# Optimization experiments

Hardware: AMD Instinct MI355X
Metric: run time of the kernel (lower is better)

The kernel has to match this reference:

```python
import jax, jax.numpy as jnp
import numpy as np

B, S, D = 2, 2048, 2048
NH, NKV, HD = 16, 4, 128
ROPE_BASE = 10000.0
NEG = -1e9


def _rope_tables(seq_len, dim):
    inv_freq = 1.0 / ROPE_BASE ** (jnp.arange(0, dim, 2, dtype=jnp.float32) / dim)
    t = jnp.arange(seq_len, dtype=jnp.float32)
    freqs = jnp.outer(t, inv_freq)                      # [S, dim/2]
    return jnp.cos(freqs), jnp.sin(freqs)


def _apply_rope(x, cos, sin):
    # x: [B, S, H, HD]; interleaved-pair rotation matching the original module
    x1 = x[..., ::2]
    x2 = x[..., 1::2]
    c = cos[None, :, None, :]
    s = sin[None, :, None, :]
    out1 = x1 * c - x2 * s
    out2 = x1 * s + x2 * c
    return jnp.stack([out1, out2], axis=-1).reshape(x.shape)


def setup_inputs() -> dict:
    key = jax.random.key(0)
    ks = jax.random.split(key, 5)
    x = jax.random.normal(ks[0], (B, S, D), dtype=jnp.float32)
    # causal additive mask [1, 1, S, S]
    causal = jnp.tril(jnp.ones((S, S), dtype=jnp.bool_))
    mask = jnp.where(causal, 0.0, NEG).astype(jnp.float32)[None, None]
    Wq = jax.random.normal(ks[1], (D, NH * HD), dtype=jnp.float32) * (D ** -0.5)
    Wk = jax.random.normal(ks[2], (D, NKV * HD), dtype=jnp.float32) * (D ** -0.5)
    Wv = jax.random.normal(ks[3], (D, NKV * HD), dtype=jnp.float32) * (D ** -0.5)
    Wo = jax.random.normal(ks[4], (NH * HD, D), dtype=jnp.float32) * ((NH * HD) ** -0.5)
    return {"x": x, "mask": mask, "Wq": Wq, "Wk": Wk, "Wv": Wv, "Wo": Wo}


def reference(x, mask, Wq, Wk, Wv, Wo):
    b, s, _ = x.shape
    q = (x @ Wq).reshape(b, s, NH, HD)
    k = (x @ Wk).reshape(b, s, NKV, HD)
    v = (x @ Wv).reshape(b, s, NKV, HD)

    cos, sin = _rope_tables(s, HD)
    q = _apply_rope(q, cos, sin)
    k = _apply_rope(k, cos, sin)

    rep = NH // NKV
    k = jnp.repeat(k, rep, axis=2)                       # [b, s, NH, HD]
    v = jnp.repeat(v, rep, axis=2)

    q = q.transpose(0, 2, 1, 3)                          # [b, NH, s, HD]
    k = k.transpose(0, 2, 1, 3)
    v = v.transpose(0, 2, 1, 3)

    scores = jnp.einsum('bhqd,bhkd->bhqk', q, k) / jnp.sqrt(jnp.float32(HD))
    scores = scores + mask
    attn = jax.nn.softmax(scores, axis=-1)
    out = jnp.einsum('bhqk,bhkd->bhqd', attn, v)
    out = out.transpose(0, 2, 1, 3).reshape(b, s, NH * HD)
    return out @ Wo
```

## Files before the change

kernel.cpp:

```cpp
#include <hip/hip_runtime.h>
#include <stdint.h>

#define B_    2
#define S_    2048
#define D_    2048
#define NH_   16
#define NKV_  4
#define HD_   128
#define M_    (B_*S_)
#define NQKV_ 3072

typedef __bf16 bf16x8 __attribute__((ext_vector_type(8)));
typedef float  f32x4  __attribute__((ext_vector_type(4)));

__device__ __forceinline__ unsigned short f2bf(float f) {
    unsigned int u = __float_as_uint(f);
    u += 0x7fffu + ((u >> 16) & 1u);
    return (unsigned short)(u >> 16);
}

__device__ __forceinline__ void async_cp16(const unsigned short* g, unsigned short* l) {
    __builtin_amdgcn_global_load_lds((const __attribute__((address_space(1))) void*)g,
                                     (__attribute__((address_space(3))) void*)l, 16, 0, 0);
}

__global__ void cast_x(const float* __restrict__ x, unsigned short* __restrict__ xb) {
    int idx = blockIdx.x * 256 + threadIdx.x;
    float4 v = ((const float4*)x)[idx];
    unsigned int lo = (unsigned int)f2bf(v.x) | ((unsigned int)f2bf(v.y) << 16);
    unsigned int hi = (unsigned int)f2bf(v.z) | ((unsigned int)f2bf(v.w) << 16);
    ((uint2*)xb)[idx] = make_uint2(lo, hi);
}

__global__ void transpose_cast(const float* __restrict__ src,
                               unsigned short* __restrict__ dst, int ncols) {
    __shared__ float tile[32][33];
    int tx = threadIdx.x, ty = threadIdx.y;
    int n0 = blockIdx.x * 32, k0 = blockIdx.y * 32;
#pragma unroll
    for (int i = 0; i < 4; i++) {
        int k = k0 + ty + i * 8;
        tile[ty + i * 8][tx] = src[(long)k * ncols + n0 + tx];
    }
    __syncthreads();
#pragma unroll
    for (int i = 0; i < 4; i++) {
        int n = n0 + ty + i * 8;
        dst[(long)n * 2048 + k0 + tx] = f2bf(tile[tx][ty + i * 8]);
    }
}

__global__ void rope_tables(float2* __restrict__ ctab) {
    int gid = blockIdx.x * 256 + threadIdx.x;
    int s = gid >> 6, i = gid & 63;
    float inv = exp2f(-(float)i * 0.20762050593046014f);
    float ang = (float)s * inv;
    float sn, cs; sincosf(ang, &sn, &cs);
    ctab[gid] = make_float2(cs, sn);
}


__device__ __forceinline__ bf16x8 lds_frag(const unsigned short* hb, int r, int ks, int quad) {
    int p = (r * 128 + ks * 64 + quad * 16) ^ ((r & 4) << 3);
    return *(const bf16x8*)((const char*)hb + p);
}

__device__ __forceinline__ void stage_half(const unsigned short* g, int Kel,
                                           unsigned short* lhalf, int wid, int lane) {
#pragma unroll
    for (int i = 0; i < 2; i++) {
        int chunk = wid * 2 + i;
        int o = chunk * 1024 + lane * 16;
        int row = o >> 7;
        int cb = (o & 127) ^ ((row & 4) << 3);
        async_cp16((const unsigned short*)((const char*)g + (size_t)row * Kel * 2 + cb),
                   lhalf + chunk * 512);
    }
}

template<int MB, int NB>
__device__ __forceinline__ void cluster(f32x4 (*acc)[4], bf16x8 (*a)[2], bf16x8 (*b)[2]) {
    __builtin_amdgcn_sched_barrier(0);
    __builtin_amdgcn_s_barrier();
    asm volatile("s_waitcnt lgkmcnt(0)" ::: "memory");
    __builtin_amdgcn_sched_barrier(0);
    __builtin_amdgcn_s_setprio(1);
#pragma unroll
    for (int ks = 0; ks < 2; ks++)
#pragma unroll
        for (int mi = 0; mi < 4; mi++)
#pragma unroll
            for (int ni = 0; ni < 2; ni++)
                acc[MB + mi][NB + ni] = __builtin_amdgcn_mfma_f32_16x16x32_bf16(
                    a[mi][ks], b[ni][ks], acc[MB + mi][NB + ni], 0, 0, 0);
    __builtin_amdgcn_s_setprio(0);
    __builtin_amdgcn_sched_barrier(0);
    __builtin_amdgcn_s_barrier();
    __builtin_amdgcn_sched_barrier(0);
}

__device__ __forceinline__ void gemm256_core(const unsigned short* __restrict__ A,
                                             const unsigned short* __restrict__ Bt,
                                             const int K, const int m0, const int n0,
                                             char* sm, f32x4 (*acc)[4]) {
    const int tid  = threadIdx.x;
    const int lane = tid & 63, wid = tid >> 6;
    const int quad = lane >> 4, l16 = lane & 15;
    const int wm = wid >> 2, wn = wid & 3;

    unsigned short* sA00 = (unsigned short*)(sm);
    unsigned short* sA01 = (unsigned short*)(sm + 16384);
    unsigned short* sA10 = (unsigned short*)(sm + 32768);
    unsigned short* sA11 = (unsigned short*)(sm + 49152);
    unsigned short* sB00 = (unsigned short*)(sm + 65536);
    unsigned short* sB01 = (unsigned short*)(sm + 81920);
    unsigned short* sB10 = (unsigned short*)(sm + 98304);
    unsigned short* sB11 = (unsigned short*)(sm + 114688);

    const unsigned short* A0 = A  + (size_t)m0 * K;
    const unsigned short* A1 = A  + (size_t)(m0 + 128) * K;
    const unsigned short* B0 = Bt + (size_t)n0 * K;
    const unsigned short* B1 = Bt + (size_t)(n0 + 128) * K;

    stage_half(A0,      K, sA00, wid, lane);
    stage_half(B1,      K, sB01, wid, lane);
    stage_half(A1,      K, sA01, wid, lane);
    stage_half(B0,      K, sB00, wid, lane);
    __builtin_amdgcn_sched_barrier(0);
    stage_half(A0 + 64, K, sA10, wid, lane);
    stage_half(B1 + 64, K, sB11, wid, lane);
    stage_half(A1 + 64, K, sA11, wid, lane);
    asm volatile("s_waitcnt vmcnt(6)" ::: "memory");
    __builtin_amdgcn_sched_barrier(0);
    __builtin_amdgcn_s_barrier();
    __builtin_amdgcn_sched_barrier(0);

    const int NIT = K >> 7;
    for (int j = 0; j < NIT; ++j) {
        const bool st = (j < NIT - 1);
        const int kof1 = (2 * j + 1) * 64;
        const int kof2 = (2 * j + 2) * 64;
        const int kof3 = (2 * j + 3) * 64;
        bf16x8 af[4][2], bA[2][2], bB[2][2];

#pragma unroll
        for (int mi = 0; mi < 4; mi++)
#pragma unroll
            for (int ks = 0; ks < 2; ks++)
                af[mi][ks] = lds_frag(sA00, wm * 64 + mi * 16 + l16, ks, quad);
#pragma unroll
        for (int ni = 0; ni < 2; ni++)
#pragma unroll
            for (int ks = 0; ks < 2; ks++)
                bA[ni][ks] = lds_frag(sB00, wn * 32 + ni * 16 + l16, ks, quad);
        stage_half(B0 + kof1, K, sB10, wid, lane);
        cluster<0, 0>(acc, af, bA);

#pragma unroll
        for (int ni = 0; ni < 2; ni++)
#pragma unroll
            for (int ks = 0; ks < 2; ks++)
                bB[ni][ks] = lds_frag(sB01, wn * 32 + ni * 16 + l16, ks, quad);
        if (st) stage_half(A0 + kof2, K, sA00, wid, lane);
        cluster<0, 2>(acc, af, bB);

#pragma unroll
        for (int mi = 0; mi < 4; mi++)
#pragma unroll
            for (int ks = 0; ks < 2; ks++)
                af[mi][ks] = lds_frag(sA01, wm * 64 + mi * 16 + l16, ks, quad);
        if (st) stage_half(B1 + kof2, K, sB01, wid, lane);
        cluster<4, 2>(acc, af, bB);

#pragma unroll
        for (int ni = 0; ni < 2; ni++)
#pragma unroll
            for (int ks = 0; ks < 2; ks++)
                bA[ni][ks] = lds_frag(sB00, wn * 32 + ni * 16 + l16, ks, quad);
        if (st) {
            stage_half(A1 + kof2, K, sA01, wid, lane);
            asm volatile("s_waitcnt vmcnt(6)" ::: "memory");
        } else {
            asm volatile("s_waitcnt vmcnt(0)" ::: "memory");
        }
        cluster<4, 0>(acc, af, bA);

#pragma unroll
        for (int mi = 0; mi < 4; mi++)
#pragma unroll
            for (int ks = 0; ks < 2; ks++)
                af[mi][ks] = lds_frag(sA10, wm * 64 + mi * 16 + l16, ks, quad);
#pragma unroll
        for (int ni = 0; ni < 2; ni++)
#pragma unroll
            for (int ks = 0; ks < 2; ks++)
                bA[ni][ks] = lds_frag(sB10, wn * 32 + ni * 16 + l16, ks, quad);
        if (st) stage_half(B0 + kof2, K, sB00, wid, lane);
        cluster<0, 0>(acc, af, bA);

#pragma unroll
        for (int ni = 0; ni < 2; ni++)
#pragma unroll
            for (int ks = 0; ks < 2; ks++)
                bB[ni][ks] = lds_frag(sB11, wn * 32 + ni * 16 + l16, ks, quad);
        if (st) stage_half(A0 + kof3, K, sA10, wid, lane);
        cluster<0, 2>(acc, af, bB);

#pragma unroll
        for (int mi = 0; mi < 4; mi++)
#pragma unroll
            for (int ks = 0; ks < 2; ks++)
                af[mi][ks] = lds_frag(sA11, wm * 64 + mi * 16 + l16, ks, quad);
        if (st) stage_half(B1 + kof3, K, sB11, wid, lane);
        cluster<4, 2>(acc, af, bB);

#pragma unroll
        for (int ni = 0; ni < 2; ni++)
#pragma unroll
            for (int ks = 0; ks < 2; ks++)
                bA[ni][ks] = lds_frag(sB10, wn * 32 + ni * 16 + l16, ks, quad);
        if (st) {
            stage_half(A1 + kof3, K, sA11, wid, lane);
            asm volatile("s_waitcnt vmcnt(6)" ::: "memory");
        }
        cluster<4, 0>(acc, af, bA);
    }
}

__global__ __launch_bounds__(512, 2) void gemm_qkv256(const unsigned short* __restrict__ A,
                                                      const unsigned short* __restrict__ Bt,
                                                      const float2* __restrict__ ctab,
                                                      unsigned short* __restrict__ Qr,
                                                      unsigned short* __restrict__ Kr,
                                                      unsigned short* __restrict__ Vrow) {
    extern __shared__ char sm[];
    const int m0 = blockIdx.y * 256, n0 = blockIdx.x * 256;
    f32x4 acc[8][4] = {};
    gemm256_core(A, Bt, D_, m0, n0, sm, acc);

    const int tid  = threadIdx.x;
    const int lane = tid & 63, wid = tid >> 6;
    const int quad = lane >> 4, l16 = lane & 15;
    const int wm = wid >> 2, wn = wid & 3;

    if (n0 < 2048) {
#pragma unroll
        for (int mt = 0; mt < 8; mt++) {
            int rowb = m0 + ((mt & 4) << 5) + wm * 64 + (mt & 3) * 16 + quad * 4;
#pragma unroll
            for (int nt = 0; nt < 4; nt++) {
                int col = n0 + ((nt & 2) << 6) + wn * 32 + (nt & 1) * 16 + l16;
                int h = col >> 7, d = col & 127;
#pragma unroll
                for (int r = 0; r < 4; r++) {
                    int row = rowb + r;
                    int s = row & 2047, b = row >> 11;
                    float2 cs = ctab[s * 64 + (d >> 1)];
                    float own = acc[mt][nt][r];
                    float other = __shfl_xor(own, 1);
                    float val = (d & 1) ? (other * cs.y + own * cs.x)
                                        : (own * cs.x - other * cs.y);
                    Qr[((size_t)(b * 16 + h) * 2048 + s) * 128 + d] = f2bf(val);
                }
            }
        }
    } else if (n0 < 2560) {
#pragma unroll
        for (int mt = 0; mt < 8; mt++) {
            int rowb = m0 + ((mt & 4) << 5) + wm * 64 + (mt & 3) * 16 + quad * 4;
#pragma unroll
            for (int nt = 0; nt < 4; nt++) {
                int col = n0 + ((nt & 2) << 6) + wn * 32 + (nt & 1) * 16 + l16;
                int kvh = (col - 2048) >> 7, d = col & 127;
#pragma unroll
                for (int r = 0; r < 4; r++) {
                    int row = rowb + r;
                    int s = row & 2047, b = row >> 11;
                    float2 cs = ctab[s * 64 + (d >> 1)];
                    float own = acc[mt][nt][r];
                    float other = __shfl_xor(own, 1);
                    float val = (d & 1) ? (other * cs.y + own * cs.x)
                                        : (own * cs.x - other * cs.y);
                    Kr[((size_t)(b * 4 + kvh) * 2048 + s) * 128 + d] = f2bf(val);
                }
            }
        }
    } else {
#pragma unroll
        for (int mt = 0; mt < 8; mt++) {
            int rowb = m0 + ((mt & 4) << 5) + wm * 64 + (mt & 3) * 16 + quad * 4;
#pragma unroll
            for (int nt = 0; nt < 4; nt++) {
                int col = n0 + ((nt & 2) << 6) + wn * 32 + (nt & 1) * 16 + l16;
#pragma unroll
                for (int r = 0; r < 4; r++)
                    Vrow[(size_t)(rowb + r) * 512 + (col - 2560)] = f2bf(acc[mt][nt][r]);
            }
        }
    }
}

__global__ __launch_bounds__(512, 2) void gemm_bt256(const unsigned short* __restrict__ A,
                                                     const unsigned short* __restrict__ Bt,
                                                     float* __restrict__ C) {
    extern __shared__ char sm[];
    const int m0 = blockIdx.y * 256, n0 = blockIdx.x * 256;
    f32x4 acc[8][4] = {};
    gemm256_core(A, Bt, NH_ * HD_, m0, n0, sm, acc);

    const int tid  = threadIdx.x;
    const int lane = tid & 63, wid = tid >> 6;
    const int quad = lane >> 4, l16 = lane & 15;
    const int wm = wid >> 2, wn = wid & 3;
#pragma unroll
    for (int mt = 0; mt < 8; mt++) {
        int rowb = m0 + ((mt & 4) << 5) + wm * 64 + (mt & 3) * 16 + quad * 4;
#pragma unroll
        for (int nt = 0; nt < 4; nt++) {
            int col = n0 + ((nt & 2) << 6) + wn * 32 + (nt & 1) * 16 + l16;
#pragma unroll
            for (int r = 0; r < 4; r++)
                C[(size_t)(rowb + r) * 2048 + col] = acc[mt][nt][r];
        }
    }
}

__global__ void v_trans_bf(const unsigned short* __restrict__ Vrow,
                           unsigned short* __restrict__ Vt) {
    __shared__ unsigned short tile[32][34];
    int tx = threadIdx.x, ty = threadIdx.y;
    int s0 = blockIdx.x * 32, d0 = blockIdx.y * 32;
    int bz = blockIdx.z;
    int b = bz >> 2, kvh = bz & 3;
#pragma unroll
    for (int i = 0; i < 4; i++) {
        int s = s0 + ty + i * 8;
        tile[ty + i * 8][tx] = Vrow[(long)(b * 2048 + s) * 512 + kvh * 128 + d0 + tx];
    }
    __syncthreads();
#pragma unroll
    for (int i = 0; i < 4; i++) {
        int d = d0 + ty + i * 8;
        Vt[((long)bz * 128 + d) * 2048 + s0 + tx] = tile[tx][ty + i * 8];
    }
}

__global__ __launch_bounds__(256) void attn_fwd(const unsigned short* __restrict__ Qr,
                                                const unsigned short* __restrict__ Kr,
                                                const unsigned short* __restrict__ Vt,
                                                unsigned short* __restrict__ O) {
    __shared__ unsigned short Ks[64][136];
    __shared__ unsigned short Vs[128][72];
    __shared__ unsigned short Ps[4][16][72];
    const int tid  = threadIdx.x;
    const int lane = tid & 63, wid = tid >> 6;
    const int quad = lane >> 4, l16 = lane & 15;
    const int pid = blockIdx.x, h = blockIdx.y, b = blockIdx.z;
    const int kvh = h >> 2;
    const unsigned short* qp = Qr + (long)(b * NH_ + h) * S_ * HD_;
    const unsigned short* kp = Kr + (long)(b * NKV_ + kvh) * S_ * HD_;
    const unsigned short* vp = Vt + (long)(b * NKV_ + kvh) * HD_ * S_;
    const float sc2 = 0.08838834764831845f * 1.4426950408889634f;

    bf16x8 ones;
#pragma unroll
    for (int i = 0; i < 8; i++) ones[i] = (__bf16)1.0f;

    for (int phase = 0; phase < 2; phase++) {
        const int qt = phase ? pid : 31 - pid;
        const int qw = qt * 64 + wid * 16;

        bf16x8 aq[4];
#pragma unroll
        for (int ks = 0; ks < 4; ks++)
            aq[ks] = *(const bf16x8*)&qp[(long)(qw + l16) * HD_ + ks * 32 + quad * 8];

        f32x4 o[8] = {};
        float mi[4], li[4];
#pragma unroll
        for (int r = 0; r < 4; r++) { mi[r] = -3.0e38f; li[r] = 0.f; }

        for (int kt = 0; kt <= qt; kt++) {
            const int kv0 = kt * 64;
            __syncthreads();
#pragma unroll
            for (int i = 0; i < 4; i++) {
                int idx = tid + i * 256;
                int row = idx >> 4, c = (idx & 15) * 8;
                *(uint4*)&Ks[row][c] = *(const uint4*)&kp[(long)(kv0 + row) * HD_ + c];
            }
#pragma unroll
            for (int i = 0; i < 4; i++) {
                int idx = tid + i * 256;
                int hd = idx >> 3, c = (idx & 7) * 8;
                *(uint4*)&Vs[hd][c] = *(const uint4*)&vp[(long)hd * S_ + kv0 + c];
            }
            __syncthreads();

            f32x4 s[4] = {};
#pragma unroll
            for (int ks = 0; ks < 4; ks++)
#pragma unroll
                for (int nt = 0; nt < 4; nt++) {
                    bf16x8 kb = *(const bf16x8*)&Ks[nt * 16 + l16][ks * 32 + quad * 8];
                    s[nt] = __builtin_amdgcn_mfma_f32_16x16x32_bf16(aq[ks], kb, s[nt], 0, 0, 0);
                }

            float mt[4];
#pragma unroll
            for (int r = 0; r < 4; r++) mt[r] = -3.0e38f;
            if (kv0 + 63 > qw) {
#pragma unroll
                for (int nt = 0; nt < 4; nt++) {
                    int kvp = kv0 + nt * 16 + l16;
#pragma unroll
                    for (int r = 0; r < 4; r++) {
                        float sv = s[nt][r] * sc2;
                        sv = (kvp <= qw + quad * 4 + r) ? sv : -1.0e30f;
                        s[nt][r] = sv;
                        mt[r] = fmaxf(mt[r], sv);
                    }
                }
            } else {
#pragma unroll
                for (int nt = 0; nt < 4; nt++)
#pragma unroll
                    for (int r = 0; r < 4; r++) {
                        float sv = s[nt][r] * sc2;
                        s[nt][r] = sv;
                        mt[r] = fmaxf(mt[r], sv);
                    }
            }
#pragma unroll
            for (int off = 1; off < 16; off <<= 1)
#pragma unroll
                for (int r = 0; r < 4; r++)
                    mt[r] = fmaxf(mt[r], __shfl_xor(mt[r], off));
            float al[4];
#pragma unroll
            for (int r = 0; r < 4; r++) {
                float mn = fmaxf(mi[r], mt[r]);
                al[r] = exp2f(mi[r] - mn);
                mi[r] = mn;
            }
#pragma unroll
            for (int nt = 0; nt < 4; nt++)
#pragma unroll
                for (int r = 0; r < 4; r++)
                    s[nt][r] = exp2f(s[nt][r] - mi[r]);
#pragma unroll
            for (int t = 0; t < 8; t++)
#pragma unroll
                for (int r = 0; r < 4; r++) o[t][r] *= al[r];

#pragma unroll
            for (int nt = 0; nt < 4; nt++)
#pragma unroll
                for (int r = 0; r < 4; r++)
                    Ps[wid][quad * 4 + r][nt * 16 + l16] = f2bf(s[nt][r]);

            f32x4 sumf = {};
#pragma unroll
            for (int ks2 = 0; ks2 < 2; ks2++) {
                bf16x8 pa = *(const bf16x8*)&Ps[wid][l16][ks2 * 32 + quad * 8];
                sumf = __builtin_amdgcn_mfma_f32_16x16x32_bf16(pa, ones, sumf, 0, 0, 0);
#pragma unroll
                for (int vt = 0; vt < 8; vt++) {
                    bf16x8 vb = *(const bf16x8*)&Vs[vt * 16 + l16][ks2 * 32 + quad * 8];
                    o[vt] = __builtin_amdgcn_mfma_f32_16x16x32_bf16(pa, vb, o[vt], 0, 0, 0);
                }
            }
#pragma unroll
            for (int r = 0; r < 4; r++) li[r] = li[r] * al[r] + sumf[r];
        }

#pragma unroll
        for (int r = 0; r < 4; r++) {
            float inv_l = 1.0f / li[r];
            int qpos = qw + quad * 4 + r;
#pragma unroll
            for (int vt = 0; vt < 8; vt++) {
                float val = o[vt][r] * inv_l;
                O[(long)(b * S_ + qpos) * 2048 + h * 128 + vt * 16 + l16] = f2bf(val);
            }
        }
    }
}

extern "C" void kernel_launch(void* const* d_in, const int* in_sizes, int n_in,
                              void* d_out, int out_size, void* d_ws, size_t ws_size,
                              hipStream_t stream) {
    const float* x  = (const float*)d_in[0];
    const float* Wq = (const float*)d_in[2];
    const float* Wk = (const float*)d_in[3];
    const float* Wv = (const float*)d_in[4];
    const float* Wo = (const float*)d_in[5];

    char* ws = (char*)d_ws;
    unsigned short* xb    = (unsigned short*)(ws);
    unsigned short* Wqkvt = (unsigned short*)(ws + 16777216);
    unsigned short* Wot   = (unsigned short*)(ws + 29360128);
    float2*         ctab  = (float2*)        (ws + 37748736);
    unsigned short* Qr    = (unsigned short*)(ws + 38797312);
    unsigned short* Kr    = (unsigned short*)(ws + 55574528);
    unsigned short* Vrow  = (unsigned short*)(ws + 59768832);
    unsigned short* Vt    = (unsigned short*)(ws + 63963136);
    unsigned short* attn  = (unsigned short*)(ws + 68157440);

    static int attr_set = 0;
    if (!attr_set) {
        hipFuncSetAttribute(reinterpret_cast<const void*>(gemm_qkv256),
                            hipFuncAttributeMaxDynamicSharedMemorySize, 131072);
        hipFuncSetAttribute(reinterpret_cast<const void*>(gemm_bt256),
                            hipFuncAttributeMaxDynamicSharedMemorySize, 131072);
        attr_set = 1;
    }

    cast_x<<<8192, 256, 0, stream>>>(x, xb);
    dim3 tb(32, 8);
    transpose_cast<<<dim3(64, 64), tb, 0, stream>>>(Wq, Wqkvt, 2048);
    transpose_cast<<<dim3(16, 64), tb, 0, stream>>>(Wk, Wqkvt + 2048 * 2048, 512);
    transpose_cast<<<dim3(16, 64), tb, 0, stream>>>(Wv, Wqkvt + 2560 * 2048, 512);
    transpose_cast<<<dim3(64, 64), tb, 0, stream>>>(Wo, Wot, 2048);
    rope_tables<<<512, 256, 0, stream>>>(ctab);

    gemm_qkv256<<<dim3(12, 16), 512, 131072, stream>>>(xb, Wqkvt, ctab, Qr, Kr, Vrow);

    v_trans_bf<<<dim3(64, 4, 8), tb, 0, stream>>>(Vrow, Vt);

    attn_fwd<<<dim3(16, NH_, B_), 256, 0, stream>>>(Qr, Kr, Vt, attn);

    gemm_bt256<<<dim3(8, 16), 512, 131072, stream>>>(attn, Wot, (float*)d_out);
}
```

Before: 369.9 us.

## Load K/V tiles with async global-to-LDS copies using XOR-swizzled layout

Replaces the register-staged K and V tile loads in the attention kernel with direct global_load_lds copies into unpadded LDS tiles. An XOR swizzle on the source address replaces the old row padding to avoid bank conflicts. It precomputes per-thread source, destination and read pointers, and skips the rescale of the O accumulator and row sum when no row maximum grew anywhere in the wavefront. It also switches the bf16 conversion to the hardware cast. The async copies are still bracketed by the same barriers, so they do not overlap with compute, and correctness depends on the swizzle matching between the copy and the reads.

```diff
diff --git a/kernel.cpp b/kernel.cpp
--- a/kernel.cpp
+++ b/kernel.cpp
@@ -17,6 +17,11 @@
     unsigned int u = __float_as_uint(f);
     u += 0x7fffu + ((u >> 16) & 1u);
     return (unsigned short)(u >> 16);
+}
+
+__device__ __forceinline__ unsigned short cvt_bf(float f) {
+    __bf16 b = (__bf16)f;
+    return *(unsigned short*)&b;
 }
 
 __device__ __forceinline__ void async_cp16(const unsigned short* g, unsigned short* l) {
@@ -349,8 +354,8 @@
                                                 const unsigned short* __restrict__ Kr,
                                                 const unsigned short* __restrict__ Vt,
                                                 unsigned short* __restrict__ O) {
-    __shared__ unsigned short Ks[64][136];
-    __shared__ unsigned short Vs[128][72];
+    __shared__ unsigned short Ks[64 * 128];
+    __shared__ unsigned short Vs[128 * 64];
     __shared__ unsigned short Ps[4][16][72];
     const int tid  = threadIdx.x;
     const int lane = tid & 63, wid = tid >> 6;
@@ -362,6 +367,33 @@
     const unsigned short* vp = Vt + (long)(b * NKV_ + kvh) * HD_ * S_;
     const float sc2 = 0.08838834764831845f * 1.4426950408889634f;
 
+    const char* ksrc[4]; unsigned short* kdst[4];
+    const char* vsrc[4]; unsigned short* vdst[4];
+#pragma unroll
+    for (int i = 0; i < 4; i++) {
+        int o = (i * 256 + tid) * 16;
+        {
+            int row = o >> 8, col = o & 255;
+            int cb = col ^ ((row & 7) << 4);
+            ksrc[i] = (const char*)kp + (size_t)row * 256 + cb;
+            kdst[i] = (unsigned short*)((char*)Ks + o);
+        }
+        {
+            int row = o >> 7, col = o & 127;
+            int cb = col ^ ((row & 7) << 4);
+            vsrc[i] = (const char*)vp + (size_t)row * (S_ * 2) + cb;
+            vdst[i] = (unsigned short*)((char*)Vs + o);
+        }
+    }
+    const char* kaP[4];
+#pragma unroll
+    for (int ks = 0; ks < 4; ks++)
+        kaP[ks] = (const char*)Ks + l16 * 256 + ((ks * 64 + quad * 16) ^ ((l16 & 7) << 4));
+    const char* vaP[2];
+#pragma unroll
+    for (int ks2 = 0; ks2 < 2; ks2++)
+        vaP[ks2] = (const char*)Vs + l16 * 128 + ((ks2 * 64 + quad * 16) ^ ((l16 & 7) << 4));
+
     bf16x8 ones;
 #pragma unroll
     for (int i = 0; i < 8; i++) ones[i] = (__bf16)1.0f;
@@ -384,17 +416,11 @@
             const int kv0 = kt * 64;
             __syncthreads();
 #pragma unroll
-            for (int i = 0; i < 4; i++) {
-                int idx = tid + i * 256;
-                int row = idx >> 4, c = (idx & 15) * 8;
-                *(uint4*)&Ks[row][c] = *(const uint4*)&kp[(long)(kv0 + row) * HD_ + c];
-            }
-#pragma unroll
-            for (int i = 0; i < 4; i++) {
-                int idx = tid + i * 256;
-                int hd = idx >> 3, c = (idx & 7) * 8;
-                *(uint4*)&Vs[hd][c] = *(const uint4*)&vp[(long)hd * S_ + kv0 + c];
-            }
+            for (int i = 0; i < 4; i++)
+                async_cp16((const unsigned short*)(ksrc[i] + (size_t)kv0 * 256), kdst[i]);
+#pragma unroll
+            for (int i = 0; i < 4; i++)
+                async_cp16((const unsigned short*)(vsrc[i] + (size_t)kv0 * 2), vdst[i]);
             __syncthreads();
 
             f32x4 s[4] = {};
@@ -402,13 +428,13 @@
             for (int ks = 0; ks < 4; ks++)
 #pragma unroll
                 for (int nt = 0; nt < 4; nt++) {
-                    bf16x8 kb = *(const bf16x8*)&Ks[nt * 16 + l16][ks * 32 + quad * 8];
+                    bf16x8 kb = *(const bf16x8*)(kaP[ks] + nt * 4096);
                     s[nt] = __builtin_amdgcn_mfma_f32_16x16x32_bf16(aq[ks], kb, s[nt], 0, 0, 0);
                 }
 
-            float mt[4];
-#pragma unroll
-            for (int r = 0; r < 4; r++) mt[r] = -3.0e38f;
+            float mt4[4];
+#pragma unroll
+            for (int r = 0; r < 4; r++) mt4[r] = -3.0e38f;
             if (kv0 + 63 > qw) {
 #pragma unroll
                 for (int nt = 0; nt < 4; nt++) {
@@ -418,7 +444,7 @@
                         float sv = s[nt][r] * sc2;
                         sv = (kvp <= qw + quad * 4 + r) ? sv : -1.0e30f;
                         s[nt][r] = sv;
-                        mt[r] = fmaxf(mt[r], sv);
+                        mt4[r] = fmaxf(mt4[r], sv);
                     }
                 }
             } else {
@@ -428,36 +454,43 @@
                     for (int r = 0; r < 4; r++) {
                         float sv = s[nt][r] * sc2;
                         s[nt][r] = sv;
-                        mt[r] = fmaxf(mt[r], sv);
+                        mt4[r] = fmaxf(mt4[r], sv);
                     }
             }
 #pragma unroll
             for (int off = 1; off < 16; off <<= 1)
 #pragma unroll
                 for (int r = 0; r < 4; r++)
-                    mt[r] = fmaxf(mt[r], __shfl_xor(mt[r], off));
+                    mt4[r] = fmaxf(mt4[r], __shfl_xor(mt4[r], off));
+
+            bool grew = false;
+#pragma unroll
+            for (int r = 0; r < 4; r++) grew |= (mt4[r] > mi[r]);
             float al[4];
-#pragma unroll
-            for (int r = 0; r < 4; r++) {
-                float mn = fmaxf(mi[r], mt[r]);
-                al[r] = exp2f(mi[r] - mn);
-                mi[r] = mn;
+            const bool resc = __any(grew);
+            if (resc) {
+#pragma unroll
+                for (int r = 0; r < 4; r++) {
+                    float mn = fmaxf(mi[r], mt4[r]);
+                    al[r] = exp2f(mi[r] - mn);
+                    mi[r] = mn;
+                }
+#pragma unroll
+                for (int t = 0; t < 8; t++)
+#pragma unroll
+                    for (int r = 0; r < 4; r++) o[t][r] *= al[r];
             }
 #pragma unroll
             for (int nt = 0; nt < 4; nt++)
 #pragma unroll
                 for (int r = 0; r < 4; r++)
                     s[nt][r] = exp2f(s[nt][r] - mi[r]);
-#pragma unroll
-            for (int t = 0; t < 8; t++)
-#pragma unroll
-                for (int r = 0; r < 4; r++) o[t][r] *= al[r];
 
 #pragma unroll
             for (int nt = 0; nt < 4; nt++)
 #pragma unroll
                 for (int r = 0; r < 4; r++)
-                    Ps[wid][quad * 4 + r][nt * 16 + l16] = f2bf(s[nt][r]);
+                    Ps[wid][quad * 4 + r][nt * 16 + l16] = cvt_bf(s[nt][r]);
 
             f32x4 sumf = {};
 #pragma unroll
@@ -466,12 +499,17 @@
                 sumf = __builtin_amdgcn_mfma_f32_16x16x32_bf16(pa, ones, sumf, 0, 0, 0);
 #pragma unroll
                 for (int vt = 0; vt < 8; vt++) {
-                    bf16x8 vb = *(const bf16x8*)&Vs[vt * 16 + l16][ks2 * 32 + quad * 8];
+                    bf16x8 vb = *(const bf16x8*)(vaP[ks2] + vt * 2048);
                     o[vt] = __builtin_amdgcn_mfma_f32_16x16x32_bf16(pa, vb, o[vt], 0, 0, 0);
                 }
             }
-#pragma unroll
-            for (int r = 0; r < 4; r++) li[r] = li[r] * al[r] + sumf[r];
+            if (resc) {
+#pragma unroll
+                for (int r = 0; r < 4; r++) li[r] = li[r] * al[r] + sumf[r];
+            } else {
+#pragma unroll
+                for (int r = 0; r < 4; r++) li[r] += sumf[r];
+            }
         }
 
 #pragma unroll
@@ -481,7 +519,7 @@
 #pragma unroll
             for (int vt = 0; vt < 8; vt++) {
                 float val = o[vt][r] * inv_l;
-                O[(long)(b * S_ + qpos) * 2048 + h * 128 + vt * 16 + l16] = f2bf(val);
+                O[(long)(b * S_ + qpos) * 2048 + h * 128 + vt * 16 + l16] = cvt_bf(val);
             }
         }
     }
```

New measurement: 422.0 us. +14.1%, slower.
